# Optimization experiments

Measured on AMD Instinct MI355X. Metric: run time of the kernel, lower is better.

The kernel has to match this reference:

```python
import jax, jax.numpy as jnp
import numpy as np

HDIM = 1024
CDIM = 256
TEMPER = 10.0
IGNORE_OUT = 0.0
EPS = 1e-6


def setup_inputs() -> dict:
    key = jax.random.key(0)
    ks = jax.random.split(key, 6)
    B, T, D = 2, 128, 384
    x = jax.random.normal(ks[0], (B, T, D), jnp.float32)
    y = jax.random.normal(ks[1], (B, T, D), jnp.float32)
    # xavier-normal style init for the two linear layers
    W_enc = jax.random.normal(ks[2], (D, HDIM), jnp.float32) * np.sqrt(2.0 / (D + HDIM))
    b_enc = jnp.zeros((HDIM,), jnp.float32)
    W_dec = jax.random.normal(ks[3], (HDIM, D), jnp.float32) * np.sqrt(2.0 / (D + HDIM))
    b_dec = jnp.zeros((D,), jnp.float32)
    return {"x": x, "y": y, "W_enc": W_enc, "b_enc": b_enc, "W_dec": W_dec, "b_dec": b_dec}


def reference(x, y, W_enc, b_enc, W_dec, b_dec):
    B, T, D = x.shape
    n_iter = HDIM // CDIM
    pad = D - 1
    # shift_idx[s, j] = s + j : window of width D at offset s, s in [0, 2D-2]
    shift_idx = jnp.arange(2 * D - 1)[:, None] + jnp.arange(D)[None, :]

    seq_mask = (y == IGNORE_OUT)                       # (B,T,D) bool
    denom_seq = jnp.sum(~seq_mask).astype(x.dtype)
    qn = jnp.linalg.norm(y, axis=-1)                   # (B,T)

    mask_prev = None
    x_dis, losses = [], []
    for _ in range(n_iter):
        # --- _pad_for_shift: (B,T,2D-1,D) shifted windows of x ---
        kp = jnp.pad(x, ((0, 0), (0, 0), (pad, pad)))  # (B,T,3D-2)
        kpt = kp[..., shift_idx]                       # (B,T,2D-1,D)
        # --- _score (cos) + argmax over shifts ---
        kn = jnp.linalg.norm(kpt, axis=-1)             # (B,T,2D-1)
        sim = jnp.einsum('btsd,btd->bts', kpt, y) / (qn[..., None] * kn + EPS)
        sim = jnp.where(jnp.isnan(sim), 0.0, sim)
        theta = jnp.argmax(sim, axis=-1)               # (B,T) int
        x_opt = jnp.take_along_axis(kpt, theta[..., None, None], axis=-2)[..., 0, :]  # (B,T,D)
        # --- attention: elementwise cos-scaled score, temp softmax, detached ---
        dn = (jnp.linalg.norm(x_opt, axis=-1, keepdims=True)
              * jnp.linalg.norm(y, axis=-1, keepdims=True) + EPS)
        attn = jax.nn.softmax((x_opt * y / dn) / TEMPER, axis=-1)
        attn = jnp.where(jnp.isnan(attn), 0.0, attn)
        attn = jax.lax.stop_gradient(attn)
        x_attn = x_opt * attn
        # --- _reverse_pad_for_shift: window at offset 2D-2-theta ---
        kp2 = jnp.pad(x_attn, ((0, 0), (0, 0), (pad, pad)))
        rev_idx = (2 * D - 2 - theta)[..., None] + jnp.arange(D)  # (B,T,D)
        x_ele = jnp.take_along_axis(kp2, rev_idx, axis=-1)         # (B,T,D)
        # --- self_net: encoder -> top-k sparsify -> decoder_self ---
        h = x_ele @ W_enc + b_enc                      # (B,T,HDIM)
        if mask_prev is not None:
            h = jnp.where(mask_prev > 0, 1e-10, h)
        _, idx_top = jax.lax.top_k(h, CDIM)            # (B,T,CDIM)
        flat = idx_top.reshape(B * T, CDIM)
        mask_cur = jnp.zeros((B * T, HDIM), x.dtype).at[
            jnp.arange(B * T)[:, None], flat].set(1.0).reshape(B, T, HDIM)
        if mask_prev is None:
            mask_prev = mask_cur
        else:
            mask_prev = mask_prev + mask_cur - mask_prev * mask_cur
        h = h * mask_cur
        out = h @ W_dec + b_dec                        # (B,T,D)
        x_dis.append(out)
        # --- SeqLoss (masked MSE, mean-reduced by count of valid elems) ---
        err = jnp.where(seq_mask, 0.0, (out - x) ** 2) / denom_seq
        losses.append(jnp.sum(err))
    return jnp.stack(x_dis), jnp.stack(losses)
```

## Files before the change

### kernel.cpp

```cpp
#include <hip/hip_runtime.h>
#include <math.h>

#define DD 384
#define HD 1024
#define CD 256
#define NS 765
#define NITER 4
#define NROWS 256
#define TEMPER_F 10.0f
#define EPSF 1e-6f
#define CUTF 1e-10f
#define XSTR 1156

typedef unsigned long long u64;
typedef unsigned int u32;

__device__ __forceinline__ u32 flipf(float f) {
    u32 u = __float_as_uint(f);
    return u ^ ((u32)((int)u >> 31) | 0x80000000u);
}
__device__ __forceinline__ float unflipf(u32 s) {
    u32 fl = ~s;
    u32 u = (fl & 0x80000000u) ? (fl ^ 0x80000000u) : ~fl;
    return __uint_as_float(u);
}

__global__ __launch_bounds__(512) void fused_kernel(
    const float* __restrict__ x, const float* __restrict__ y,
    const float* __restrict__ Wenc, const float* __restrict__ benc,
    const float* __restrict__ Wdec, const float* __restrict__ bdec,
    float* __restrict__ out_xdis, float* __restrict__ lossp,
    int* __restrict__ ycnt)
{
    const int row  = blockIdx.x;
    const int tid  = threadIdx.x;
    const int lane = tid & 63;
    const int wid  = tid >> 6;

    __shared__ float xp[4][XSTR];
    __shared__ float yr[DD];
    __shared__ float xa[DD];
    __shared__ float xe_s[DD];
    __shared__ u64   skey[HD];
    __shared__ uint2 dec2[HD];
    __shared__ float wred[8];
    __shared__ int   wredi[8];
    __shared__ float s_sc[4];
    __shared__ int   s_theta, s_fb;
    __shared__ float loss4[NITER];

    const float* xrow = x + row * DD;
    const float* yrow = y + row * DD;

    for (int i = tid; i < XSTR; i += 512) {
#pragma unroll
        for (int r = 0; r < 4; ++r) {
            int t = i + r;
            xp[r][i] = (t >= DD - 1 && t < 2 * DD - 1) ? xrow[t - (DD - 1)] : 0.f;
        }
    }
    if (tid < DD) yr[tid] = yrow[tid];
    __syncthreads();

    if (tid < DD) {
        float p = yr[tid] * yr[tid];
        for (int o = 32; o; o >>= 1) p += __shfl_xor(p, o, 64);
        if (lane == 0) wred[wid] = p;
    }
    __syncthreads();
    if (tid == 0) {
        float s = 0.f;
        for (int w = 0; w < 6; ++w) s += wred[w];
        s_sc[0] = sqrtf(s);
    }
    __syncthreads();
    const float qn = s_sc[0];

    const float* xps = xp[tid & 3];
    const int a1 = tid & ~3;
    float bv; int bs;
    if (tid < NS - 512) {
        float dot1 = 0.f, nrm1 = 0.f, dot2 = 0.f, nrm2 = 0.f;
#pragma unroll 4
        for (int j = 0; j < DD; j += 4) {
            float4 yv = *(const float4*)&yr[j];
            float4 x1 = *(const float4*)&xps[a1 + j];
            float4 x2 = *(const float4*)&xps[a1 + 512 + j];
            dot1 += x1.x * yv.x; nrm1 += x1.x * x1.x;
            dot1 += x1.y * yv.y; nrm1 += x1.y * x1.y;
            dot1 += x1.z * yv.z; nrm1 += x1.z * x1.z;
            dot1 += x1.w * yv.w; nrm1 += x1.w * x1.w;
            dot2 += x2.x * yv.x; nrm2 += x2.x * x2.x;
            dot2 += x2.y * yv.y; nrm2 += x2.y * x2.y;
            dot2 += x2.z * yv.z; nrm2 += x2.z * x2.z;
            dot2 += x2.w * yv.w; nrm2 += x2.w * x2.w;
        }
        float sim1 = dot1 / (qn * sqrtf(nrm1) + EPSF);
        float sim2 = dot2 / (qn * sqrtf(nrm2) + EPSF);
        bv = sim1; bs = tid;
        if (sim2 > bv) { bv = sim2; bs = tid + 512; }
    } else {
        float dot1 = 0.f, nrm1 = 0.f;
#pragma unroll 4
        for (int j = 0; j < DD; j += 4) {
            float4 yv = *(const float4*)&yr[j];
            float4 x1 = *(const float4*)&xps[a1 + j];
            dot1 += x1.x * yv.x; nrm1 += x1.x * x1.x;
            dot1 += x1.y * yv.y; nrm1 += x1.y * x1.y;
            dot1 += x1.z * yv.z; nrm1 += x1.z * x1.z;
            dot1 += x1.w * yv.w; nrm1 += x1.w * x1.w;
        }
        bv = dot1 / (qn * sqrtf(nrm1) + EPSF);
        bs = tid;
    }
    for (int o = 32; o; o >>= 1) {
        float v2 = __shfl_xor(bv, o, 64);
        int   i2 = __shfl_xor(bs, o, 64);
        if (v2 > bv || (v2 == bv && i2 < bs)) { bv = v2; bs = i2; }
    }
    if (lane == 0) { wred[wid] = bv; wredi[wid] = bs; }
    __syncthreads();
    if (tid == 0) {
        float v = wred[0]; int b = wredi[0];
        for (int w = 1; w < 8; ++w)
            if (wred[w] > v || (wred[w] == v && wredi[w] < b)) { v = wred[w]; b = wredi[w]; }
        s_theta = b;
    }
    __syncthreads();
    const int theta = s_theta;

    float xo = 0.f;
    if (tid < DD) {
        xo = xp[theta & 3][(theta & ~3) + tid];
        float p = xo * xo;
        for (int o = 32; o; o >>= 1) p += __shfl_xor(p, o, 64);
        if (lane == 0) wred[wid] = p;
    }
    __syncthreads();
    if (tid == 0) {
        float s = 0.f;
        for (int w = 0; w < 6; ++w) s += wred[w];
        s_sc[1] = sqrtf(s) * qn + EPSF;
    }
    __syncthreads();
    float z = 0.f;
    if (tid < DD) {
        z = (xo * yr[tid] / s_sc[1]) / TEMPER_F;
        float m = z;
        for (int o = 32; o; o >>= 1) { float w2 = __shfl_xor(m, o, 64); if (w2 > m) m = w2; }
        if (lane == 0) wred[wid] = m;
    }
    __syncthreads();
    if (tid == 0) {
        float m = wred[0];
        for (int w = 1; w < 6; ++w) if (wred[w] > m) m = wred[w];
        s_sc[2] = m;
    }
    __syncthreads();
    float ez = 0.f;
    if (tid < DD) {
        ez = expf(z - s_sc[2]);
        float p = ez;
        for (int o = 32; o; o >>= 1) p += __shfl_xor(p, o, 64);
        if (lane == 0) wred[wid] = p;
    }
    __syncthreads();
    if (tid == 0) {
        float s = 0.f;
        for (int w = 0; w < 6; ++w) s += wred[w];
        s_sc[3] = s;
    }
    __syncthreads();
    if (tid < DD) {
        xa[tid] = xo * (ez / s_sc[3]);
        int c = (yr[tid] != 0.f) ? 1 : 0;
        for (int o = 32; o; o >>= 1) c += __shfl_xor(c, o, 64);
        if (lane == 0) wredi[wid] = c;
    }
    __syncthreads();
    if (tid == 0) {
        int s = 0;
        for (int w = 0; w < 6; ++w) s += wredi[w];
        ycnt[row] = s;
    }
    if (tid < DD) {
        int sj = tid - (theta - (DD - 1));
        xe_s[tid] = (sj >= 0 && sj < DD) ? xa[sj] : 0.f;
    }
    __syncthreads();

    float h0 = benc[tid], h1 = benc[tid + 512];
    const float* w0 = Wenc + tid;
#pragma unroll 4
    for (int j = 0; j < DD; j += 4) {
        float4 xv = *(const float4*)&xe_s[j];
        h0 += xv.x * w0[(j + 0) * HD];       h1 += xv.x * w0[(j + 0) * HD + 512];
        h0 += xv.y * w0[(j + 1) * HD];       h1 += xv.y * w0[(j + 1) * HD + 512];
        h0 += xv.z * w0[(j + 2) * HD];       h1 += xv.z * w0[(j + 2) * HD + 512];
        h0 += xv.w * w0[(j + 3) * HD];       h1 += xv.w * w0[(j + 3) * HD + 512];
    }
    skey[tid]       = ((u64)(~flipf(h0)) << 32) | (u32)tid;
    skey[tid + 512] = ((u64)(~flipf(h1)) << 32) | (u32)(tid + 512);
    if (tid == 0) s_fb = HD;
    if (tid < NITER) loss4[tid] = 0.f;
    __syncthreads();

    bool prevc = false;
    for (int k = 2; k <= HD; k <<= 1) {
        for (int j = k >> 1; j > 0; j >>= 1) {
            if (j >= 128 || prevc) __syncthreads();
            else __builtin_amdgcn_wave_barrier();
            const int low = tid & (j - 1);
            const int i   = ((tid - low) << 1) + low;
            const int p   = i + j;
            u64 a = skey[i], b = skey[p];
            const bool up = ((i & k) == 0);
            if (up ? (a > b) : (a < b)) { skey[i] = b; skey[p] = a; }
            prevc = (j >= 128);
        }
    }
    __syncthreads();

    int fbloc = HD;
#pragma unroll
    for (int u = 0; u < 2; ++u) {
        int pos = tid + u * 512;
        u64 kk = skey[pos];
        float v = unflipf((u32)(kk >> 32));
        u32 idx = (u32)kk;
        dec2[pos] = make_uint2(__float_as_uint(v), idx * DD);
        if (!(v > CUTF) && pos < fbloc) fbloc = pos;
    }
    for (int o = 32; o; o >>= 1) { int t2 = __shfl_xor(fbloc, o, 64); if (t2 < fbloc) fbloc = t2; }
    if (lane == 0) atomicMin(&s_fb, fbloc);
    __syncthreads();
    const int fb = s_fb;

#pragma unroll
    for (int u = 0; u < 3; ++u) {
        const int gi = u * 512 + tid;
        const int k  = gi / DD;
        const int d  = gi - k * DD;
        int n = (k == 0) ? CD : fb - k * CD;
        if (n < 0) n = 0; if (n > CD) n = CD;
        float acc = bdec[d];
        const float* wd = Wdec + d;
        const int base = k * CD;
        int r = 0;
        for (; r + 8 <= n; r += 8) {
#pragma unroll
            for (int q = 0; q < 8; q += 2) {
                uint4 dv = *(const uint4*)&dec2[base + r + q];
                acc += __uint_as_float(dv.x) * wd[dv.y];
                acc += __uint_as_float(dv.z) * wd[dv.w];
            }
        }
        for (; r < n; ++r) {
            uint2 dv = dec2[base + r];
            acc += __uint_as_float(dv.x) * wd[dv.y];
        }
        out_xdis[((size_t)k * NROWS + row) * DD + d] = acc;
        float e = acc - xrow[d];
        float l = (yr[d] != 0.f) ? e * e : 0.f;
        for (int o = 32; o; o >>= 1) l += __shfl_xor(l, o, 64);
        if (lane == 0) atomicAdd(&loss4[k], l);
    }
    __syncthreads();
    if (tid < NITER) lossp[row * NITER + tid] = loss4[tid];
}

__global__ __launch_bounds__(256) void finalize2(
    const float* __restrict__ lossp, const int* __restrict__ ycnt,
    float* __restrict__ losses)
{
    const int tid = threadIdx.x, lane = tid & 63, w = tid >> 6;
    __shared__ int ctot[4];
    int c = ycnt[tid];
    for (int o = 32; o; o >>= 1) c += __shfl_xor(c, o, 64);
    if (lane == 0) ctot[w] = c;
    __syncthreads();
    const int total = ctot[0] + ctot[1] + ctot[2] + ctot[3];
    float s = lossp[lane * NITER + w] + lossp[(lane + 64) * NITER + w]
            + lossp[(lane + 128) * NITER + w] + lossp[(lane + 192) * NITER + w];
    for (int o = 32; o; o >>= 1) s += __shfl_xor(s, o, 64);
    if (lane == 0) losses[w] = s / (float)total;
}

extern "C" void kernel_launch(void* const* d_in, const int* in_sizes, int n_in,
                              void* d_out, int out_size, void* d_ws, size_t ws_size,
                              hipStream_t stream) {
    const float* x    = (const float*)d_in[0];
    const float* y    = (const float*)d_in[1];
    const float* Wenc = (const float*)d_in[2];
    const float* benc = (const float*)d_in[3];
    const float* Wdec = (const float*)d_in[4];
    const float* bdec = (const float*)d_in[5];

    float* out  = (float*)d_out;
    float* loss = out + (out_size - NITER);

    float* lossp = (float*)d_ws;
    int*   ycnt  = (int*)(lossp + NROWS * NITER);

    fused_kernel<<<NROWS, 512, 0, stream>>>(x, y, Wenc, benc, Wdec, bdec,
                                            out, lossp, ycnt);
    finalize2<<<1, 256, 0, stream>>>(lossp, ycnt, loss);
}
```

Before: 123.9 us.

## Register-blocked shift scoring, float4 encoder/decoder, padded sort keys

```diff
diff --git a/kernel.cpp b/kernel.cpp
--- a/kernel.cpp
+++ b/kernel.cpp
@@ -10,7 +10,8 @@
 #define TEMPER_F 10.0f
 #define EPSF 1e-6f
 #define CUTF 1e-10f
-#define XSTR 1156
+#define XPLEN 1152
+#define SKLEN (HD + (HD>>4))
 
 typedef unsigned long long u64;
 typedef unsigned int u32;
@@ -24,6 +25,7 @@
     u32 u = (fl & 0x80000000u) ? (fl ^ 0x80000000u) : ~fl;
     return __uint_as_float(u);
 }
+__device__ __forceinline__ int phys(int i) { return i + (i >> 4); }
 
 __global__ __launch_bounds__(512) void fused_kernel(
     const float* __restrict__ x, const float* __restrict__ y,
@@ -37,14 +39,16 @@
     const int lane = tid & 63;
     const int wid  = tid >> 6;
 
-    __shared__ float xp[4][XSTR];
-    __shared__ float yr[DD];
+    __shared__ __align__(16) float xpad[XPLEN];
+    __shared__ __align__(16) float yr[DD];
     __shared__ float xa[DD];
-    __shared__ float xe_s[DD];
-    __shared__ u64   skey[HD];
-    __shared__ uint2 dec2[HD];
+    __shared__ __align__(16) float xe_s[DD];
+    __shared__ __align__(16) float hpart[HD];
+    __shared__ u64   skey[SKLEN];
+    __shared__ __align__(16) uint2 dec2[HD];
     __shared__ float wred[8];
     __shared__ int   wredi[8];
+    __shared__ float wredn[8];
     __shared__ float s_sc[4];
     __shared__ int   s_theta, s_fb;
     __shared__ float loss4[NITER];
@@ -52,13 +56,8 @@
     const float* xrow = x + row * DD;
     const float* yrow = y + row * DD;
 
-    for (int i = tid; i < XSTR; i += 512) {
-#pragma unroll
-        for (int r = 0; r < 4; ++r) {
-            int t = i + r;
-            xp[r][i] = (t >= DD - 1 && t < 2 * DD - 1) ? xrow[t - (DD - 1)] : 0.f;
-        }
-    }
+    for (int i = tid; i < XPLEN; i += 512)
+        xpad[i] = (i >= DD - 1 && i < 2 * DD - 1) ? xrow[i - (DD - 1)] : 0.f;
     if (tid < DD) yr[tid] = yrow[tid];
     __syncthreads();
 
@@ -76,76 +75,62 @@
     __syncthreads();
     const float qn = s_sc[0];
 
-    const float* xps = xp[tid & 3];
-    const int a1 = tid & ~3;
-    float bv; int bs;
-    if (tid < NS - 512) {
-        float dot1 = 0.f, nrm1 = 0.f, dot2 = 0.f, nrm2 = 0.f;
+    float bv = -INFINITY; int bs = 0x7fffffff; float bn = 0.f;
+    if (tid < 192) {
+        const float4* xp4 = (const float4*)xpad;
+        const float4* yp4 = (const float4*)yr;
+        float4 A = xp4[tid];
+        const float f0 = A.x * A.x, f1 = A.y * A.y, f2 = A.z * A.z;
+        float d0 = 0.f, d1 = 0.f, d2 = 0.f, d3 = 0.f, n0 = 0.f;
 #pragma unroll 4
-        for (int j = 0; j < DD; j += 4) {
-            float4 yv = *(const float4*)&yr[j];
-            float4 x1 = *(const float4*)&xps[a1 + j];
-            float4 x2 = *(const float4*)&xps[a1 + 512 + j];
-            dot1 += x1.x * yv.x; nrm1 += x1.x * x1.x;
-            dot1 += x1.y * yv.y; nrm1 += x1.y * x1.y;
-            dot1 += x1.z * yv.z; nrm1 += x1.z * x1.z;
-            dot1 += x1.w * yv.w; nrm1 += x1.w * x1.w;
-            dot2 += x2.x * yv.x; nrm2 += x2.x * x2.x;
-            dot2 += x2.y * yv.y; nrm2 += x2.y * x2.y;
-            dot2 += x2.z * yv.z; nrm2 += x2.z * x2.z;
-            dot2 += x2.w * yv.w; nrm2 += x2.w * x2.w;
-        }
-        float sim1 = dot1 / (qn * sqrtf(nrm1) + EPSF);
-        float sim2 = dot2 / (qn * sqrtf(nrm2) + EPSF);
-        bv = sim1; bs = tid;
-        if (sim2 > bv) { bv = sim2; bs = tid + 512; }
-    } else {
-        float dot1 = 0.f, nrm1 = 0.f;
-#pragma unroll 4
-        for (int j = 0; j < DD; j += 4) {
-            float4 yv = *(const float4*)&yr[j];
-            float4 x1 = *(const float4*)&xps[a1 + j];
-            dot1 += x1.x * yv.x; nrm1 += x1.x * x1.x;
-            dot1 += x1.y * yv.y; nrm1 += x1.y * x1.y;
-            dot1 += x1.z * yv.z; nrm1 += x1.z * x1.z;
-            dot1 += x1.w * yv.w; nrm1 += x1.w * x1.w;
-        }
-        bv = dot1 / (qn * sqrtf(nrm1) + EPSF);
-        bs = tid;
+        for (int jc = 0; jc < 96; ++jc) {
+            float4 B = xp4[tid + jc + 1];
+            float4 Y = yp4[jc];
+            d0 += A.x * Y.x; d0 += A.y * Y.y; d0 += A.z * Y.z; d0 += A.w * Y.w;
+            d1 += A.y * Y.x; d1 += A.z * Y.y; d1 += A.w * Y.z; d1 += B.x * Y.w;
+            d2 += A.z * Y.x; d2 += A.w * Y.y; d2 += B.x * Y.z; d2 += B.y * Y.w;
+            d3 += A.w * Y.x; d3 += B.x * Y.y; d3 += B.y * Y.z; d3 += B.z * Y.w;
+            n0 += A.x * A.x; n0 += A.y * A.y; n0 += A.z * A.z; n0 += A.w * A.w;
+            A = B;
+        }
+        const float n1 = n0 - f0 + A.x * A.x;
+        const float n2 = n1 - f1 + A.y * A.y;
+        const float n3 = n2 - f2 + A.z * A.z;
+        const int s0 = 4 * tid;
+        float sim0 = d0 / (qn * sqrtf(n0) + EPSF);
+        float sim1 = d1 / (qn * sqrtf(n1) + EPSF);
+        float sim2 = d2 / (qn * sqrtf(n2) + EPSF);
+        float sim3 = d3 / (qn * sqrtf(n3) + EPSF);
+        bv = sim0; bs = s0; bn = n0;
+        if (s0 + 1 < NS && sim1 > bv) { bv = sim1; bs = s0 + 1; bn = n1; }
+        if (s0 + 2 < NS && sim2 > bv) { bv = sim2; bs = s0 + 2; bn = n2; }
+        if (s0 + 3 < NS && sim3 > bv) { bv = sim3; bs = s0 + 3; bn = n3; }
     }
     for (int o = 32; o; o >>= 1) {
         float v2 = __shfl_xor(bv, o, 64);
         int   i2 = __shfl_xor(bs, o, 64);
-        if (v2 > bv || (v2 == bv && i2 < bs)) { bv = v2; bs = i2; }
-    }
-    if (lane == 0) { wred[wid] = bv; wredi[wid] = bs; }
-    __syncthreads();
-    if (tid == 0) {
-        float v = wred[0]; int b = wredi[0];
+        float n2 = __shfl_xor(bn, o, 64);
+        if (v2 > bv || (v2 == bv && i2 < bs)) { bv = v2; bs = i2; bn = n2; }
+    }
+    if (lane == 0) { wred[wid] = bv; wredi[wid] = bs; wredn[wid] = bn; }
+    __syncthreads();
+    if (tid == 0) {
+        float v = wred[0]; int b = wredi[0]; float nn = wredn[0];
         for (int w = 1; w < 8; ++w)
-            if (wred[w] > v || (wred[w] == v && wredi[w] < b)) { v = wred[w]; b = wredi[w]; }
+            if (wred[w] > v || (wred[w] == v && wredi[w] < b)) {
+                v = wred[w]; b = wredi[w]; nn = wredn[w];
+            }
         s_theta = b;
+        s_sc[1] = sqrtf(nn) * qn + EPSF;
     }
     __syncthreads();
     const int theta = s_theta;
-
-    float xo = 0.f;
-    if (tid < DD) {
-        xo = xp[theta & 3][(theta & ~3) + tid];
-        float p = xo * xo;
-        for (int o = 32; o; o >>= 1) p += __shfl_xor(p, o, 64);
-        if (lane == 0) wred[wid] = p;
-    }
-    __syncthreads();
-    if (tid == 0) {
-        float s = 0.f;
-        for (int w = 0; w < 6; ++w) s += wred[w];
-        s_sc[1] = sqrtf(s) * qn + EPSF;
-    }
-    __syncthreads();
-    float z = 0.f;
-    if (tid < DD) {
-        z = (xo * yr[tid] / s_sc[1]) / TEMPER_F;
+    const float dn = s_sc[1];
+
+    float xo = 0.f, z = 0.f;
+    if (tid < DD) {
+        xo = xpad[theta + tid];
+        z = (xo * yr[tid] / dn) / TEMPER_F;
         float m = z;
         for (int o = 32; o; o >>= 1) { float w2 = __shfl_xor(m, o, 64); if (w2 > m) m = w2; }
         if (lane == 0) wred[wid] = m;
@@ -189,20 +174,37 @@
     }
     __syncthreads();
 
-    float h0 = benc[tid], h1 = benc[tid + 512];
-    const float* w0 = Wenc + tid;
+    const int c4 = tid & 255;
+    const int jh = tid >> 8;
+    float4 acc = make_float4(0.f, 0.f, 0.f, 0.f);
+    {
+        const float* wbase = Wenc + (size_t)(jh * 192) * HD + 4 * c4;
+        const float* xb = xe_s + jh * 192;
 #pragma unroll 4
-    for (int j = 0; j < DD; j += 4) {
-        float4 xv = *(const float4*)&xe_s[j];
-        h0 += xv.x * w0[(j + 0) * HD];       h1 += xv.x * w0[(j + 0) * HD + 512];
-        h0 += xv.y * w0[(j + 1) * HD];       h1 += xv.y * w0[(j + 1) * HD + 512];
-        h0 += xv.z * w0[(j + 2) * HD];       h1 += xv.z * w0[(j + 2) * HD + 512];
-        h0 += xv.w * w0[(j + 3) * HD];       h1 += xv.w * w0[(j + 3) * HD + 512];
-    }
-    skey[tid]       = ((u64)(~flipf(h0)) << 32) | (u32)tid;
-    skey[tid + 512] = ((u64)(~flipf(h1)) << 32) | (u32)(tid + 512);
+        for (int j = 0; j < 192; ++j) {
+            float xv = xb[j];
+            float4 w = *(const float4*)(wbase + (size_t)j * HD);
+            acc.x += xv * w.x; acc.y += xv * w.y;
+            acc.z += xv * w.z; acc.w += xv * w.w;
+        }
+    }
+    if (jh == 1) *(float4*)&hpart[4 * c4] = acc;
     if (tid == 0) s_fb = HD;
     if (tid < NITER) loss4[tid] = 0.f;
+    __syncthreads();
+    if (jh == 0) {
+        float4 hp = *(const float4*)&hpart[4 * c4];
+        float4 bb = *(const float4*)&benc[4 * c4];
+        float hv0 = acc.x + hp.x + bb.x;
+        float hv1 = acc.y + hp.y + bb.y;
+        float hv2 = acc.z + hp.z + bb.z;
+        float hv3 = acc.w + hp.w + bb.w;
+        const int col = 4 * c4;
+        skey[phys(col + 0)] = ((u64)(~flipf(hv0)) << 32) | (u32)(col + 0);
+        skey[phys(col + 1)] = ((u64)(~flipf(hv1)) << 32) | (u32)(col + 1);
+        skey[phys(col + 2)] = ((u64)(~flipf(hv2)) << 32) | (u32)(col + 2);
+        skey[phys(col + 3)] = ((u64)(~flipf(hv3)) << 32) | (u32)(col + 3);
+    }
     __syncthreads();
 
     bool prevc = false;
@@ -213,9 +215,10 @@
             const int low = tid & (j - 1);
             const int i   = ((tid - low) << 1) + low;
             const int p   = i + j;
-            u64 a = skey[i], b = skey[p];
+            const int pi = phys(i), pp = phys(p);
+            u64 a = skey[pi], b = skey[pp];
             const bool up = ((i & k) == 0);
-            if (up ? (a > b) : (a < b)) { skey[i] = b; skey[p] = a; }
+            if (up ? (a > b) : (a < b)) { skey[pi] = b; skey[pp] = a; }
             prevc = (j >= 128);
         }
     }
@@ -223,9 +226,9 @@
 
     int fbloc = HD;
 #pragma unroll
-    for (int u = 0; u < 2; ++u) {
-        int pos = tid + u * 512;
-        u64 kk = skey[pos];
+    for (int u2 = 0; u2 < 2; ++u2) {
+        int pos = tid + u2 * 512;
+        u64 kk = skey[phys(pos)];
         float v = unflipf((u32)(kk >> 32));
         u32 idx = (u32)kk;
         dec2[pos] = make_uint2(__float_as_uint(v), idx * DD);
@@ -236,32 +239,49 @@
     __syncthreads();
     const int fb = s_fb;
 
-#pragma unroll
-    for (int u = 0; u < 3; ++u) {
-        const int gi = u * 512 + tid;
-        const int k  = gi / DD;
-        const int d  = gi - k * DD;
-        int n = (k == 0) ? CD : fb - k * CD;
-        if (n < 0) n = 0; if (n > CD) n = CD;
-        float acc = bdec[d];
-        const float* wd = Wdec + d;
+    {
+        const int k  = tid >> 7;
+        const int g  = tid & 127;
+        const bool active = (g < 96);
+        int n = 0;
+        if (active) {
+            n = (k == 0) ? CD : fb - k * CD;
+            if (n < 0) n = 0; if (n > CD) n = CD;
+        }
+        float4 oacc = make_float4(0.f, 0.f, 0.f, 0.f);
+        if (active) oacc = *(const float4*)&bdec[4 * g];
+        const float* wd = Wdec + 4 * g;
         const int base = k * CD;
         int r = 0;
-        for (; r + 8 <= n; r += 8) {
-#pragma unroll
-            for (int q = 0; q < 8; q += 2) {
-                uint4 dv = *(const uint4*)&dec2[base + r + q];
-                acc += __uint_as_float(dv.x) * wd[dv.y];
-                acc += __uint_as_float(dv.z) * wd[dv.w];
-            }
-        }
-        for (; r < n; ++r) {
+        for (; r + 2 <= n; r += 2) {
+            uint4 dv = *(const uint4*)&dec2[base + r];
+            float v0 = __uint_as_float(dv.x);
+            float4 w0 = *(const float4*)(wd + dv.y);
+            float v1 = __uint_as_float(dv.z);
+            float4 w1 = *(const float4*)(wd + dv.w);
+            oacc.x += v0 * w0.x; oacc.y += v0 * w0.y;
+            oacc.z += v0 * w0.z; oacc.w += v0 * w0.w;
+            oacc.x += v1 * w1.x; oacc.y += v1 * w1.y;
+            oacc.z += v1 * w1.z; oacc.w += v1 * w1.w;
+        }
+        if (r < n) {
             uint2 dv = dec2[base + r];
-            acc += __uint_as_float(dv.x) * wd[dv.y];
-        }
-        out_xdis[((size_t)k * NROWS + row) * DD + d] = acc;
-        float e = acc - xrow[d];
-        float l = (yr[d] != 0.f) ? e * e : 0.f;
+            float v0 = __uint_as_float(dv.x);
+            float4 w0 = *(const float4*)(wd + dv.y);
+            oacc.x += v0 * w0.x; oacc.y += v0 * w0.y;
+            oacc.z += v0 * w0.z; oacc.w += v0 * w0.w;
+        }
+        float l = 0.f;
+        if (active) {
+            *(float4*)&out_xdis[((size_t)k * NROWS + row) * DD + 4 * g] = oacc;
+            float4 xv = *(const float4*)&xrow[4 * g];
+            float4 yv = *(const float4*)&yr[4 * g];
+            float e;
+            e = oacc.x - xv.x; if (yv.x != 0.f) l += e * e;
+            e = oacc.y - xv.y; if (yv.y != 0.f) l += e * e;
+            e = oacc.z - xv.z; if (yv.z != 0.f) l += e * e;
+            e = oacc.w - xv.w; if (yv.w != 0.f) l += e * e;
+        }
         for (int o = 32; o; o >>= 1) l += __shfl_xor(l, o, 64);
         if (lane == 0) atomicAdd(&loss4[k], l);
     }
```

Result: faster. 118.5 us (-4.3%).
